# Kernel optimization log

Measured on AMD Instinct MI355X. Metric: run time of the kernel, lower is better.

## Reference

```python
import jax, jax.numpy as jnp
import numpy as np

N = 50000      # nodes
E = 400000     # edges (before self-loops)
F = 128        # num_features
H = 8          # heads
C = 64         # hidden_channels (per-head dim of conv1)
K = 32         # num_classes (per-head dim of conv2)
NEG_SLOPE = 0.2


def _glorot(key, shape):
    fan_in, fan_out = shape[0], shape[-1]
    scale = jnp.sqrt(2.0 / (fan_in + fan_out)).astype(jnp.float32)
    return jax.random.normal(key, shape, dtype=jnp.float32) * scale


def setup_inputs() -> dict:
    key = jax.random.key(0)
    ks = jax.random.split(key, 14)
    return {
        "x": jax.random.normal(ks[0], (N, F), dtype=jnp.float32),
        "edge_index": jax.random.randint(ks[1], (2, E), 0, N, dtype=jnp.int32),
        "xyz": jax.random.normal(ks[2], (N, 3), dtype=jnp.float32),
        # lin1 residual: Linear(F, K)
        "lin1_w": _glorot(ks[3], (F, K)),
        "lin1_b": jnp.zeros((K,), jnp.float32),
        # conv1: GATv2Conv(F, C, heads=8, concat=False)
        "wl1": _glorot(ks[4], (F, H * C)),
        "wr1": _glorot(ks[5], (F, H * C)),
        "att1": _glorot(ks[6], (H, C)),
        "b1": jnp.zeros((C,), jnp.float32),
        # conv2: GATv2Conv(C, K, heads=8, concat=False)
        "wl2": _glorot(ks[7], (C, H * K)),
        "wr2": _glorot(ks[8], (C, H * K)),
        "att2": _glorot(ks[9], (H, K)),
        "b2": jnp.zeros((K,), jnp.float32),
    }


def _gatv2_layer(x, src, dst, wl, wr, att, bias, heads, ch):
    """GATv2Conv with concat=False (mean over heads), add_self_loops already in edges."""
    n = x.shape[0]
    xl = (x @ wl).reshape(n, heads, ch)   # source transform W_l x
    xr = (x @ wr).reshape(n, heads, ch)   # target transform W_r x
    # edge score: e_ij = a_h . leaky_relu(xl[j] + xr[i])  -> [E, H]
    e = jnp.einsum('ehc,hc->eh', jax.nn.leaky_relu(xl[src] + xr[dst], NEG_SLOPE), att)
    # segment softmax over incoming edges of each destination node
    m = jax.ops.segment_max(e, dst, num_segments=n)
    ex = jnp.exp(e - m[dst])
    denom = jax.ops.segment_sum(ex, dst, num_segments=n)
    alpha = ex / denom[dst]                                      # [E, H]
    out = jax.ops.segment_sum(alpha[:, :, None] * xl[src], dst, num_segments=n)  # [N, H, C]
    return out.mean(axis=1) + bias        # concat=False -> head average, then bias


def reference(x, edge_index, xyz, lin1_w, lin1_b, wl1, wr1, att1, b1,
              wl2, wr2, att2, b2):
    n = x.shape[0]
    # PyG GATv2Conv default: add self loops
    loops = jnp.arange(n, dtype=edge_index.dtype)
    src = jnp.concatenate([edge_index[0], loops])
    dst = jnp.concatenate([edge_index[1], loops])

    residual1 = x @ lin1_w + lin1_b                      # lin1(x)
    h = _gatv2_layer(x, src, dst, wl1, wr1, att1, b1, H, C)
    h = jax.nn.relu(h)                                   # dropout is identity in eval
    out = _gatv2_layer(h, src, dst, wl2, wr2, att2, b2, H, K)
    return out + residual1
```

## Files before the change

### kernel.cpp

```cpp
#include <hip/hip_runtime.h>
#include <hip/hip_bf16.h>

#define NNODE 50000
#define NEDGE 400000
#define NTOT  450000
#define FDIM  128
#define HEADS 8
#define SCANB ((NNODE + 255) / 256)

typedef __bf16 bf16x8 __attribute__((ext_vector_type(8)));
typedef float  f32x4  __attribute__((ext_vector_type(4)));
typedef __hip_bfloat16 bf16;

static __device__ __forceinline__ float b2f(unsigned short u) {
  union { float f; unsigned int i; } x; x.i = ((unsigned int)u) << 16; return x.f;
}

template<int CTRL>
static __device__ __forceinline__ float dpp_add(float v) {
  int x = __builtin_amdgcn_update_dpp(0, __float_as_int(v), CTRL, 0xf, 0xf, true);
  return v + __int_as_float(x);
}


__global__ __launch_bounds__(256) void k_count(const int* __restrict__ ei, int* __restrict__ deg) {
  int t = blockIdx.x * 256 + threadIdx.x;
  if (t >= NTOT) return;
  int d = (t < NEDGE) ? ei[NEDGE + t] : (t - NEDGE);
  atomicAdd(&deg[d], 1);
}

__global__ __launch_bounds__(256) void k_scan1(const int* __restrict__ deg, int* __restrict__ offs,
                                               int* __restrict__ bsum) {
  __shared__ int buf[256];
  int i = blockIdx.x * 256 + threadIdx.x;
  int v = (i < NNODE) ? deg[i] : 0;
  buf[threadIdx.x] = v;
  __syncthreads();
  for (int off = 1; off < 256; off <<= 1) {
    int t = (threadIdx.x >= off) ? buf[threadIdx.x - off] : 0;
    __syncthreads();
    buf[threadIdx.x] += t;
    __syncthreads();
  }
  if (i < NNODE) offs[i + 1] = buf[threadIdx.x];
  if (threadIdx.x == 255) bsum[blockIdx.x] = buf[255];
  if (i == 0) offs[0] = 0;
}

__global__ __launch_bounds__(256) void k_scan2(int* __restrict__ bsum, int nb) {
  __shared__ int buf[256];
  int v = (threadIdx.x < nb) ? bsum[threadIdx.x] : 0;
  buf[threadIdx.x] = v;
  __syncthreads();
  for (int off = 1; off < 256; off <<= 1) {
    int t = (threadIdx.x >= off) ? buf[threadIdx.x - off] : 0;
    __syncthreads();
    buf[threadIdx.x] += t;
    __syncthreads();
  }
  if (threadIdx.x < nb) bsum[threadIdx.x] = buf[threadIdx.x] - v;
}

__global__ __launch_bounds__(256) void k_scan3(int* __restrict__ offs, const int* __restrict__ bsum) {
  int i = blockIdx.x * 256 + threadIdx.x;
  if (i < NNODE) offs[i + 1] += bsum[blockIdx.x];
}

__global__ __launch_bounds__(256) void k_fill(const int* __restrict__ ei, const int* __restrict__ offs,
                                              int* __restrict__ cur, int* __restrict__ csrc) {
  int t = blockIdx.x * 256 + threadIdx.x;
  if (t >= NTOT) return;
  int s, d;
  if (t < NEDGE) { s = ei[t]; d = ei[NEDGE + t]; }
  else { s = t - NEDGE; d = s; }
  int pos = offs[d] + atomicAdd(&cur[d], 1);
  csrc[pos] = s;
}


__global__ __launch_bounds__(256) void k_cast(const float* __restrict__ in, bf16* __restrict__ o, int nvec) {
  int t = blockIdx.x * 256 + threadIdx.x;
  if (t >= nvec) return;
  float4 v = *(const float4*)(in + (size_t)t * 4);
  bf16* p = o + (size_t)t * 4;
  p[0] = __float2bfloat16(v.x);
  p[1] = __float2bfloat16(v.y);
  p[2] = __float2bfloat16(v.z);
  p[3] = __float2bfloat16(v.w);
}


template<int K, int N>
__global__ __launch_bounds__(256) void k_pack(const float* __restrict__ Wl, const float* __restrict__ Wr,
                                              bf16* __restrict__ Bp) {
  constexpr int KS = K / 32;
  int t = blockIdx.x * 256 + threadIdx.x;
  if (t >= (N / 16) * KS * 64) return;
  int lane = t & 63;
  int ks = (t >> 6) % KS;
  int cb = t / (64 * KS);
  int col = cb * 16 + (lane & 15);
  int k0 = ks * 32 + (lane >> 4) * 8;
  const float* W = (col < N / 2) ? Wl : Wr;
  int c = (col < N / 2) ? col : col - N / 2;
  bf16* o = Bp + (size_t)t * 8;
#pragma unroll
  for (int j = 0; j < 8; ++j)
    o[j] = __float2bfloat16(W[(size_t)(k0 + j) * (N / 2) + c]);
}


template<int K, int N>
__global__ __launch_bounds__(256) void k_mfma(const bf16* __restrict__ A,
                                              const bf16* __restrict__ Bp,
                                              bf16* __restrict__ xl, bf16* __restrict__ xr,
                                              int n) {
  constexpr int KS = K / 32;
  const int lane = threadIdx.x & 63;
  const int wave = threadIdx.x >> 6;
  const int rb = blockIdx.x * 32;
  const int cb0 = blockIdx.y * 16 + wave * 4;
  const int r16 = lane & 15, kg = lane >> 4;

  bf16x8 a[2][KS];
#pragma unroll
  for (int mf = 0; mf < 2; ++mf) {
    int row = rb + 16 * mf + r16;
    if (row >= n) row = n - 1;
    const bf16* pa = A + (size_t)row * K + kg * 8;
#pragma unroll
    for (int ks = 0; ks < KS; ++ks)
      a[mf][ks] = *(const bf16x8*)(pa + ks * 32);
  }

#pragma unroll
  for (int nf = 0; nf < 4; ++nf) {
    int cb = cb0 + nf;
    f32x4 acc0 = {0.f, 0.f, 0.f, 0.f}, acc1 = {0.f, 0.f, 0.f, 0.f};
    const bf16* pb = Bp + (size_t)cb * KS * 512 + lane * 8;
#pragma unroll
    for (int ks = 0; ks < KS; ++ks) {
      bf16x8 b = *(const bf16x8*)(pb + ks * 512);
      acc0 = __builtin_amdgcn_mfma_f32_16x16x32_bf16(a[0][ks], b, acc0, 0, 0, 0);
      acc1 = __builtin_amdgcn_mfma_f32_16x16x32_bf16(a[1][ks], b, acc1, 0, 0, 0);
    }
    int col = cb * 16 + r16;
    bf16* OUT; int c;
    if (col < N / 2) { OUT = xl; c = col; } else { OUT = xr; c = col - N / 2; }
#pragma unroll
    for (int reg = 0; reg < 4; ++reg) {
      int row0 = rb + kg * 4 + reg;
      if (row0 < n) OUT[(size_t)row0 * (N / 2) + c] = __float2bfloat16(acc0[reg]);
      int row1 = rb + 16 + kg * 4 + reg;
      if (row1 < n) OUT[(size_t)row1 * (N / 2) + c] = __float2bfloat16(acc1[reg]);
    }
  }
}


__global__ __launch_bounds__(256) void k_residual(const float* __restrict__ X,
                                                  const float* __restrict__ W,
                                                  const float* __restrict__ b,
                                                  float* __restrict__ out, int n) {
  __shared__ float xs[8 * 128];
  int row0 = blockIdx.x * 8;
  for (int t = threadIdx.x; t < 8 * 128; t += 256) {
    int r = t >> 7;
    xs[t] = (row0 + r < n) ? X[(size_t)(row0 + r) * 128 + (t & 127)] : 0.f;
  }
  __syncthreads();
  int r = threadIdx.x >> 5, c = threadIdx.x & 31;
  float acc = 0.f;
  for (int k = 0; k < 128; ++k) acc += xs[r * 128 + k] * W[k * 32 + c];
  if (row0 + r < n) out[(size_t)(row0 + r) * 32 + c] = acc + b[c];
}


template<int D, int VEC, int W, bool L1>
__global__ __launch_bounds__(64 * W, 2) void k_gat(const bf16* __restrict__ xl,
                                                   const bf16* __restrict__ xr,
                                                   const float* __restrict__ att,
                                                   const int* __restrict__ csrc,
                                                   const int* __restrict__ offs,
                                                   const float* __restrict__ bias,
                                                   const float* __restrict__ resid,
                                                   bf16* __restrict__ out1,
                                                   float* __restrict__ out2) {
  constexpr int CH = D / 8;
  constexpr int NW = VEC / 2;
  constexpr unsigned ROWB = D * 2;
  typedef unsigned int uivec __attribute__((ext_vector_type(NW)));
  __shared__ float sden[W - 1][64];
  __shared__ float sacc[W - 1][64][VEC + 1];
  const int w    = threadIdx.x >> 6;
  const int lane = threadIdx.x & 63;
  const int node = blockIdx.x;
  const int beg = offs[node], end = offs[node + 1], last = end - 1;

  const unsigned loff = (unsigned)(lane * VEC) * 2u;
  const char* xlp = (const char*)xl + loff;

  float a6[VEC], a4[VEC], xrv[VEC];
  {
    const float* pa = att + lane * VEC;
    const unsigned int* rw = (const unsigned int*)((const char*)xr + (size_t)node * ROWB + loff);
#pragma unroll
    for (int p = 0; p < NW; ++p) {
      unsigned int rv = rw[p];
      xrv[2 * p]     = __uint_as_float(rv << 16);
      xrv[2 * p + 1] = __uint_as_float(rv & 0xffff0000u);
    }
#pragma unroll
    for (int j = 0; j < VEC; ++j) {
      float a = pa[j] * 1.44269504f;
      a6[j] = 0.6f * a;
      a4[j] = 0.4f * a;
    }
  }

  float den = 0.f;
  float acc[VEC];
#pragma unroll
  for (int j = 0; j < VEC; ++j) acc[j] = 0.f;

  auto escore = [&](uivec Wd, float* av) -> float {
    float s0 = 0.f, s1 = 0.f;
#pragma unroll
    for (int p = 0; p < NW; ++p) {
      av[2 * p]     = __uint_as_float(Wd[p] << 16);
      av[2 * p + 1] = __uint_as_float(Wd[p] & 0xffff0000u);
    }
#pragma unroll
    for (int j = 0; j < VEC; ++j) {
      float t = av[j] + xrv[j];
      s0 = fmaf(a6[j], t, s0);
      s1 = fmaf(a4[j], fabsf(t), s1);
    }
    return s0 + s1;
  };

  int i = beg + w;
  if (i < end) {
    uivec A0 = *(const uivec*)(xlp + (unsigned)csrc[i] * ROWB);
    int i1 = (i + W < end) ? i + W : last;
    uivec A1 = *(const uivec*)(xlp + (unsigned)csrc[i1] * ROWB);
    for (; i + W < end; i += 2 * W) {
      int i2 = (i + 2 * W < end) ? i + 2 * W : last;
      int i3 = (i + 3 * W < end) ? i + 3 * W : last;
      uivec B0 = *(const uivec*)(xlp + (unsigned)csrc[i2] * ROWB);
      uivec B1 = *(const uivec*)(xlp + (unsigned)csrc[i3] * ROWB);

      float av0[VEC], av1[VEC];
      float s0 = escore(A0, av0);
      float s1 = escore(A1, av1);
      s0 = dpp_add<0xB1>(s0);   s1 = dpp_add<0xB1>(s1);
      s0 = dpp_add<0x4E>(s0);   s1 = dpp_add<0x4E>(s1);
      s0 = dpp_add<0x141>(s0);  s1 = dpp_add<0x141>(s1);
      float w0, w1;
      asm("v_exp_f32 %0, %1" : "=v"(w0) : "v"(s0));
      asm("v_exp_f32 %0, %1" : "=v"(w1) : "v"(s1));
      den += w0;
      den += w1;
#pragma unroll
      for (int j = 0; j < VEC; ++j) {
        acc[j] = fmaf(w0, av0[j], acc[j]);
        acc[j] = fmaf(w1, av1[j], acc[j]);
      }
      A0 = B0; A1 = B1;
    }
    if (i < end) {
      float av0[VEC];
      float s0 = escore(A0, av0);
      s0 = dpp_add<0xB1>(s0);
      s0 = dpp_add<0x4E>(s0);
      s0 = dpp_add<0x141>(s0);
      float w0;
      asm("v_exp_f32 %0, %1" : "=v"(w0) : "v"(s0));
      den += w0;
#pragma unroll
      for (int j = 0; j < VEC; ++j) acc[j] = fmaf(w0, av0[j], acc[j]);
    }
  }

  if (w > 0) {
    sden[w - 1][lane] = den;
#pragma unroll
    for (int j = 0; j < VEC; ++j) sacc[w - 1][lane][j] = acc[j];
  }
  __syncthreads();
  if (w == 0) {
#pragma unroll
    for (int ww = 0; ww < W - 1; ++ww) {
      den += sden[ww][lane];
#pragma unroll
      for (int j = 0; j < VEC; ++j) acc[j] += sacc[ww][lane][j];
    }
    const float inv = 1.f / den;
    float v[VEC];
#pragma unroll
    for (int j = 0; j < VEC; ++j) {
      float t = acc[j] * inv;
      t += __shfl_xor(t, 8);
      t += __shfl_xor(t, 16);
      t += __shfl_xor(t, 32);
      v[j] = t;
    }
    if (lane < 8) {
      int c0 = lane * VEC;
      if constexpr (L1) {
        bf16* o = out1 + (size_t)node * CH + c0;
#pragma unroll
        for (int j = 0; j < VEC; ++j) {
          float t = v[j] * 0.125f + bias[c0 + j];
          o[j] = __float2bfloat16(fmaxf(t, 0.f));
        }
      } else {
        float* o = out2 + (size_t)node * CH + c0;
        const float* rs = resid + (size_t)node * CH + c0;
#pragma unroll
        for (int j = 0; j < VEC; ++j)
          o[j] = v[j] * 0.125f + bias[c0 + j] + rs[j];
      }
    }
  }
}


extern "C" void kernel_launch(void* const* d_in, const int* in_sizes, int n_in,
                              void* d_out, int out_size, void* d_ws, size_t ws_size,
                              hipStream_t stream) {
  const float* x      = (const float*)d_in[0];
  const int*   ei     = (const int*)d_in[1];
  const float* lin1_w = (const float*)d_in[3];
  const float* lin1_b = (const float*)d_in[4];
  const float* wl1    = (const float*)d_in[5];
  const float* wr1    = (const float*)d_in[6];
  const float* att1   = (const float*)d_in[7];
  const float* b1     = (const float*)d_in[8];
  const float* wl2    = (const float*)d_in[9];
  const float* wr2    = (const float*)d_in[10];
  const float* att2   = (const float*)d_in[11];
  const float* b2     = (const float*)d_in[12];
  float* out = (float*)d_out;

  char* p = (char*)d_ws;
  auto alloc = [&](size_t bytes) {
    char* r = p;
    p += (bytes + 255) & ~size_t(255);
    return r;
  };
  int*   offs  = (int*)alloc((NNODE + 1) * 4);
  int*   deg   = (int*)alloc(NNODE * 4);
  int*   cur   = (int*)alloc(NNODE * 4);
  int*   bsum  = (int*)alloc(SCANB * 4);
  int*   csrc  = (int*)alloc((size_t)NTOT * 4);
  bf16*  xb    = (bf16*)alloc((size_t)NNODE * 128 * 2);
  bf16*  xl    = (bf16*)alloc((size_t)NNODE * 512 * 2);
  bf16*  xr    = (bf16*)alloc((size_t)NNODE * 512 * 2);
  bf16*  h1    = (bf16*)alloc((size_t)NNODE * 64 * 2);
  bf16*  Bp1   = (bf16*)alloc((size_t)128 * 1024 * 2);
  bf16*  Bp2   = (bf16*)alloc((size_t)64 * 512 * 2);
  float* resid = (float*)alloc((size_t)NNODE * 32 * 4);

  (void)hipMemsetAsync(deg, 0, NNODE * 4, stream);
  (void)hipMemsetAsync(cur, 0, NNODE * 4, stream);

  k_count<<<(NTOT + 255) / 256, 256, 0, stream>>>(ei, deg);
  k_scan1<<<SCANB, 256, 0, stream>>>(deg, offs, bsum);
  k_scan2<<<1, 256, 0, stream>>>(bsum, SCANB);
  k_scan3<<<SCANB, 256, 0, stream>>>(offs, bsum);
  k_fill<<<(NTOT + 255) / 256, 256, 0, stream>>>(ei, offs, cur, csrc);
  k_cast<<<(NNODE * 128 / 4 + 255) / 256, 256, 0, stream>>>(x, xb, NNODE * 128 / 4);
  k_pack<128, 1024><<<64, 256, 0, stream>>>(wl1, wr1, Bp1);
  k_pack<64, 512><<<16, 256, 0, stream>>>(wl2, wr2, Bp2);
  k_residual<<<NNODE / 8, 256, 0, stream>>>(x, lin1_w, lin1_b, resid, NNODE);

  k_mfma<128, 1024><<<dim3((NNODE + 31) / 32, 4), 256, 0, stream>>>(xb, Bp1, xl, xr, NNODE);
  k_gat<512, 8, 4, true><<<NNODE, 256, 0, stream>>>(xl, xr, att1, csrc, offs, b1, nullptr, h1, nullptr);

  k_mfma<64, 512><<<dim3((NNODE + 31) / 32, 2), 256, 0, stream>>>(h1, Bp2, xl, xr, NNODE);
  k_gat<256, 4, 4, false><<<NNODE, 256, 0, stream>>>(xl, xr, att2, csrc, offs, b2, resid, nullptr, out);
}
```

Baseline: 292.5 us.

## Fuse fp32-to-bf16 cast into GEMM and simplify GAT edge-index prefetch

Removes the separate cast kernel and the bf16 copy of x, converting fp32 inputs to bf16 while loading GEMM A fragments. The GAT kernel now prefetches edge source indices several iterations ahead without clamping, relying on a zero-padded tail of the CSR source array for out-of-range reads. It also splits the score dot product into independent accumulators, vectorizes the conversion helpers, and raises the occupancy hint in launch bounds from 2 to 3. The first GEMM reads twice as many A bytes per tile, and the higher occupancy hint may force register spills.

```diff
diff --git a/kernel.cpp b/kernel.cpp
--- a/kernel.cpp
+++ b/kernel.cpp
@@ -7,14 +7,11 @@
 #define FDIM  128
 #define HEADS 8
 #define SCANB ((NNODE + 255) / 256)
+#define CSRC_PAD 256
 
 typedef __bf16 bf16x8 __attribute__((ext_vector_type(8)));
 typedef float  f32x4  __attribute__((ext_vector_type(4)));
 typedef __hip_bfloat16 bf16;
-
-static __device__ __forceinline__ float b2f(unsigned short u) {
-  union { float f; unsigned int i; } x; x.i = ((unsigned int)u) << 16; return x.f;
-}
 
 template<int CTRL>
 static __device__ __forceinline__ float dpp_add(float v) {
@@ -76,18 +73,6 @@
   else { s = t - NEDGE; d = s; }
   int pos = offs[d] + atomicAdd(&cur[d], 1);
   csrc[pos] = s;
-}
-
-
-__global__ __launch_bounds__(256) void k_cast(const float* __restrict__ in, bf16* __restrict__ o, int nvec) {
-  int t = blockIdx.x * 256 + threadIdx.x;
-  if (t >= nvec) return;
-  float4 v = *(const float4*)(in + (size_t)t * 4);
-  bf16* p = o + (size_t)t * 4;
-  p[0] = __float2bfloat16(v.x);
-  p[1] = __float2bfloat16(v.y);
-  p[2] = __float2bfloat16(v.z);
-  p[3] = __float2bfloat16(v.w);
 }
 
 
@@ -111,8 +96,8 @@
 }
 
 
-template<int K, int N>
-__global__ __launch_bounds__(256) void k_mfma(const bf16* __restrict__ A,
+template<int K, int N, bool CVT>
+__global__ __launch_bounds__(256) void k_mfma(const void* __restrict__ Aptr,
                                               const bf16* __restrict__ Bp,
                                               bf16* __restrict__ xl, bf16* __restrict__ xr,
                                               int n) {
@@ -128,10 +113,25 @@
   for (int mf = 0; mf < 2; ++mf) {
     int row = rb + 16 * mf + r16;
     if (row >= n) row = n - 1;
-    const bf16* pa = A + (size_t)row * K + kg * 8;
-#pragma unroll
-    for (int ks = 0; ks < KS; ++ks)
-      a[mf][ks] = *(const bf16x8*)(pa + ks * 32);
+    if constexpr (CVT) {
+      const float* pa = (const float*)Aptr + (size_t)row * K + kg * 8;
+#pragma unroll
+      for (int ks = 0; ks < KS; ++ks) {
+        float4 f0 = *(const float4*)(pa + ks * 32);
+        float4 f1 = *(const float4*)(pa + ks * 32 + 4);
+        bf16x8 v;
+        v[0] = __float2bfloat16(f0.x); v[1] = __float2bfloat16(f0.y);
+        v[2] = __float2bfloat16(f0.z); v[3] = __float2bfloat16(f0.w);
+        v[4] = __float2bfloat16(f1.x); v[5] = __float2bfloat16(f1.y);
+        v[6] = __float2bfloat16(f1.z); v[7] = __float2bfloat16(f1.w);
+        a[mf][ks] = v;
+      }
+    } else {
+      const bf16* pa = (const bf16*)Aptr + (size_t)row * K + kg * 8;
+#pragma unroll
+      for (int ks = 0; ks < KS; ++ks)
+        a[mf][ks] = *(const bf16x8*)(pa + ks * 32);
+    }
   }
 
 #pragma unroll
@@ -178,7 +178,7 @@
 
 
 template<int D, int VEC, int W, bool L1>
-__global__ __launch_bounds__(64 * W, 2) void k_gat(const bf16* __restrict__ xl,
+__global__ __launch_bounds__(64 * W, 3) void k_gat(const bf16* __restrict__ xl,
                                                    const bf16* __restrict__ xr,
                                                    const float* __restrict__ att,
                                                    const int* __restrict__ csrc,
@@ -191,26 +191,32 @@
   constexpr int NW = VEC / 2;
   constexpr unsigned ROWB = D * 2;
   typedef unsigned int uivec __attribute__((ext_vector_type(NW)));
+  typedef float fvec __attribute__((ext_vector_type(VEC)));
   __shared__ float sden[W - 1][64];
   __shared__ float sacc[W - 1][64][VEC + 1];
   const int w    = threadIdx.x >> 6;
   const int lane = threadIdx.x & 63;
   const int node = blockIdx.x;
-  const int beg = offs[node], end = offs[node + 1], last = end - 1;
+  const int beg = offs[node], end = offs[node + 1];
 
   const unsigned loff = (unsigned)(lane * VEC) * 2u;
   const char* xlp = (const char*)xl + loff;
 
-  float a6[VEC], a4[VEC], xrv[VEC];
+  auto cvt = [](uivec Wd) -> fvec {
+    fvec r;
+#pragma unroll
+    for (int p = 0; p < NW; ++p) {
+      r[2 * p]     = __uint_as_float(Wd[p] << 16);
+      r[2 * p + 1] = __uint_as_float(Wd[p] & 0xffff0000u);
+    }
+    return r;
+  };
+
+  fvec a6, a4, xrv;
   {
     const float* pa = att + lane * VEC;
-    const unsigned int* rw = (const unsigned int*)((const char*)xr + (size_t)node * ROWB + loff);
-#pragma unroll
-    for (int p = 0; p < NW; ++p) {
-      unsigned int rv = rw[p];
-      xrv[2 * p]     = __uint_as_float(rv << 16);
-      xrv[2 * p + 1] = __uint_as_float(rv & 0xffff0000u);
-    }
+    uivec rw = *(const uivec*)((const char*)xr + (size_t)node * ROWB + loff);
+    xrv = cvt(rw);
 #pragma unroll
     for (int j = 0; j < VEC; ++j) {
       float a = pa[j] * 1.44269504f;
@@ -220,40 +226,37 @@
   }
 
   float den = 0.f;
-  float acc[VEC];
+  fvec acc;
 #pragma unroll
   for (int j = 0; j < VEC; ++j) acc[j] = 0.f;
-
-  auto escore = [&](uivec Wd, float* av) -> float {
-    float s0 = 0.f, s1 = 0.f;
-#pragma unroll
-    for (int p = 0; p < NW; ++p) {
-      av[2 * p]     = __uint_as_float(Wd[p] << 16);
-      av[2 * p + 1] = __uint_as_float(Wd[p] & 0xffff0000u);
-    }
-#pragma unroll
-    for (int j = 0; j < VEC; ++j) {
-      float t = av[j] + xrv[j];
-      s0 = fmaf(a6[j], t, s0);
-      s1 = fmaf(a4[j], fabsf(t), s1);
-    }
-    return s0 + s1;
-  };
 
   int i = beg + w;
   if (i < end) {
-    uivec A0 = *(const uivec*)(xlp + (unsigned)csrc[i] * ROWB);
-    int i1 = (i + W < end) ? i + W : last;
-    uivec A1 = *(const uivec*)(xlp + (unsigned)csrc[i1] * ROWB);
+    int c0 = csrc[i];
+    int c1 = csrc[i + W];
+    int c2 = csrc[i + 2 * W];
+    int c3 = csrc[i + 3 * W];
+    uivec A0 = *(const uivec*)(xlp + (unsigned)c0 * ROWB);
+    uivec A1 = *(const uivec*)(xlp + (unsigned)c1 * ROWB);
     for (; i + W < end; i += 2 * W) {
-      int i2 = (i + 2 * W < end) ? i + 2 * W : last;
-      int i3 = (i + 3 * W < end) ? i + 3 * W : last;
-      uivec B0 = *(const uivec*)(xlp + (unsigned)csrc[i2] * ROWB);
-      uivec B1 = *(const uivec*)(xlp + (unsigned)csrc[i3] * ROWB);
-
-      float av0[VEC], av1[VEC];
-      float s0 = escore(A0, av0);
-      float s1 = escore(A1, av1);
+      uivec B0 = *(const uivec*)(xlp + (unsigned)c2 * ROWB);
+      uivec B1 = *(const uivec*)(xlp + (unsigned)c3 * ROWB);
+      c2 = csrc[i + 4 * W];
+      c3 = csrc[i + 5 * W];
+
+      fvec av0 = cvt(A0);
+      fvec av1 = cvt(A1);
+      fvec t0 = av0 + xrv;
+      fvec t1 = av1 + xrv;
+      float s0a = 0.f, s0b = 0.f, s1a = 0.f, s1b = 0.f;
+#pragma unroll
+      for (int j = 0; j < VEC; ++j) {
+        s0a = fmaf(a6[j], t0[j], s0a);
+        s0b = fmaf(a4[j], fabsf(t0[j]), s0b);
+        s1a = fmaf(a6[j], t1[j], s1a);
+        s1b = fmaf(a4[j], fabsf(t1[j]), s1b);
+      }
+      float s0 = s0a + s0b, s1 = s1a + s1b;
       s0 = dpp_add<0xB1>(s0);   s1 = dpp_add<0xB1>(s1);
       s0 = dpp_add<0x4E>(s0);   s1 = dpp_add<0x4E>(s1);
       s0 = dpp_add<0x141>(s0);  s1 = dpp_add<0x141>(s1);
@@ -270,8 +273,15 @@
       A0 = B0; A1 = B1;
     }
     if (i < end) {
-      float av0[VEC];
-      float s0 = escore(A0, av0);
+      fvec av0 = cvt(A0);
+      fvec t0 = av0 + xrv;
+      float s0a = 0.f, s0b = 0.f;
+#pragma unroll
+      for (int j = 0; j < VEC; ++j) {
+        s0a = fmaf(a6[j], t0[j], s0a);
+        s0b = fmaf(a4[j], fabsf(t0[j]), s0b);
+      }
+      float s0 = s0a + s0b;
       s0 = dpp_add<0xB1>(s0);
       s0 = dpp_add<0x4E>(s0);
       s0 = dpp_add<0x141>(s0);
@@ -297,7 +307,7 @@
       for (int j = 0; j < VEC; ++j) acc[j] += sacc[ww][lane][j];
     }
     const float inv = 1.f / den;
-    float v[VEC];
+    fvec v;
 #pragma unroll
     for (int j = 0; j < VEC; ++j) {
       float t = acc[j] * inv;
@@ -354,8 +364,7 @@
   int*   deg   = (int*)alloc(NNODE * 4);
   int*   cur   = (int*)alloc(NNODE * 4);
   int*   bsum  = (int*)alloc(SCANB * 4);
-  int*   csrc  = (int*)alloc((size_t)NTOT * 4);
-  bf16*  xb    = (bf16*)alloc((size_t)NNODE * 128 * 2);
+  int*   csrc  = (int*)alloc(((size_t)NTOT + CSRC_PAD) * 4);
   bf16*  xl    = (bf16*)alloc((size_t)NNODE * 512 * 2);
   bf16*  xr    = (bf16*)alloc((size_t)NNODE * 512 * 2);
   bf16*  h1    = (bf16*)alloc((size_t)NNODE * 64 * 2);
@@ -365,20 +374,20 @@
 
   (void)hipMemsetAsync(deg, 0, NNODE * 4, stream);
   (void)hipMemsetAsync(cur, 0, NNODE * 4, stream);
+  (void)hipMemsetAsync(csrc + NTOT, 0, CSRC_PAD * 4, stream);
 
   k_count<<<(NTOT + 255) / 256, 256, 0, stream>>>(ei, deg);
   k_scan1<<<SCANB, 256, 0, stream>>>(deg, offs, bsum);
   k_scan2<<<1, 256, 0, stream>>>(bsum, SCANB);
   k_scan3<<<SCANB, 256, 0, stream>>>(offs, bsum);
   k_fill<<<(NTOT + 255) / 256, 256, 0, stream>>>(ei, offs, cur, csrc);
-  k_cast<<<(NNODE * 128 / 4 + 255) / 256, 256, 0, stream>>>(x, xb, NNODE * 128 / 4);
   k_pack<128, 1024><<<64, 256, 0, stream>>>(wl1, wr1, Bp1);
   k_pack<64, 512><<<16, 256, 0, stream>>>(wl2, wr2, Bp2);
   k_residual<<<NNODE / 8, 256, 0, stream>>>(x, lin1_w, lin1_b, resid, NNODE);
 
-  k_mfma<128, 1024><<<dim3((NNODE + 31) / 32, 4), 256, 0, stream>>>(xb, Bp1, xl, xr, NNODE);
+  k_mfma<128, 1024, true><<<dim3((NNODE + 31) / 32, 4), 256, 0, stream>>>(x, Bp1, xl, xr, NNODE);
   k_gat<512, 8, 4, true><<<NNODE, 256, 0, stream>>>(xl, xr, att1, csrc, offs, b1, nullptr, h1, nullptr);
 
-  k_mfma<64, 512><<<dim3((NNODE + 31) / 32, 2), 256, 0, stream>>>(h1, Bp2, xl, xr, NNODE);
+  k_mfma<64, 512, false><<<dim3((NNODE + 31) / 32, 2), 256, 0, stream>>>(h1, Bp2, xl, xr, NNODE);
   k_gat<256, 4, 4, false><<<NNODE, 256, 0, stream>>>(xl, xr, att2, csrc, offs, b2, resid, nullptr, out);
 }
```

After: 326.6 us. 1.12x slower.

## Fuse fp32-to-bf16 cast into MFMA GEMM and precompute scaled attention vectors

Applied to the files above, without the earlier changes.

Removes the separate k_cast pass over x by having the layer-1 GEMM load fp32 rows and convert them to bf16 in registers. Doubles the column fragments each wave computes (NF=8), which halves the y-grid and reuses the loaded A rows across more output columns. Adds a tiny kernel that precomputes the log2e-scaled 0.6/0.4 attention coefficients, so the GAT kernels load them as vectors instead of recomputing them per block. The trade-off is higher register pressure in the GEMM and twice the A-read bandwidth in fp32 per block.

```diff
diff --git a/kernel.cpp b/kernel.cpp
--- a/kernel.cpp
+++ b/kernel.cpp
@@ -11,10 +11,6 @@
 typedef __bf16 bf16x8 __attribute__((ext_vector_type(8)));
 typedef float  f32x4  __attribute__((ext_vector_type(4)));
 typedef __hip_bfloat16 bf16;
-
-static __device__ __forceinline__ float b2f(unsigned short u) {
-  union { float f; unsigned int i; } x; x.i = ((unsigned int)u) << 16; return x.f;
-}
 
 template<int CTRL>
 static __device__ __forceinline__ float dpp_add(float v) {
@@ -79,15 +75,19 @@
 }
 
 
-__global__ __launch_bounds__(256) void k_cast(const float* __restrict__ in, bf16* __restrict__ o, int nvec) {
+__global__ __launch_bounds__(256) void k_attp(const float* __restrict__ att1, const float* __restrict__ att2,
+                                              float* __restrict__ attp1, float* __restrict__ attp2) {
   int t = blockIdx.x * 256 + threadIdx.x;
-  if (t >= nvec) return;
-  float4 v = *(const float4*)(in + (size_t)t * 4);
-  bf16* p = o + (size_t)t * 4;
-  p[0] = __float2bfloat16(v.x);
-  p[1] = __float2bfloat16(v.y);
-  p[2] = __float2bfloat16(v.z);
-  p[3] = __float2bfloat16(v.w);
+  if (t < 512) {
+    float a = att1[t] * 1.44269504f;
+    attp1[t] = 0.6f * a;
+    attp1[512 + t] = 0.4f * a;
+  } else if (t < 768) {
+    int c = t - 512;
+    float a = att2[c] * 1.44269504f;
+    attp2[c] = 0.6f * a;
+    attp2[256 + c] = 0.4f * a;
+  }
 }
 
 
@@ -111,8 +111,8 @@
 }
 
 
-template<int K, int N>
-__global__ __launch_bounds__(256) void k_mfma(const bf16* __restrict__ A,
+template<int K, int N, int NF, bool CVT>
+__global__ __launch_bounds__(256) void k_mfma(const void* __restrict__ Aptr,
                                               const bf16* __restrict__ Bp,
                                               bf16* __restrict__ xl, bf16* __restrict__ xr,
                                               int n) {
@@ -120,7 +120,7 @@
   const int lane = threadIdx.x & 63;
   const int wave = threadIdx.x >> 6;
   const int rb = blockIdx.x * 32;
-  const int cb0 = blockIdx.y * 16 + wave * 4;
+  const int cb0 = blockIdx.y * (4 * NF) + wave * NF;
   const int r16 = lane & 15, kg = lane >> 4;
 
   bf16x8 a[2][KS];
@@ -128,14 +128,29 @@
   for (int mf = 0; mf < 2; ++mf) {
     int row = rb + 16 * mf + r16;
     if (row >= n) row = n - 1;
-    const bf16* pa = A + (size_t)row * K + kg * 8;
-#pragma unroll
-    for (int ks = 0; ks < KS; ++ks)
-      a[mf][ks] = *(const bf16x8*)(pa + ks * 32);
-  }
-
-#pragma unroll
-  for (int nf = 0; nf < 4; ++nf) {
+    if constexpr (CVT) {
+      const float* pa = (const float*)Aptr + (size_t)row * K + kg * 8;
+#pragma unroll
+      for (int ks = 0; ks < KS; ++ks) {
+        float4 f0 = *(const float4*)(pa + ks * 32);
+        float4 f1 = *(const float4*)(pa + ks * 32 + 4);
+        bf16x8 v;
+        v[0] = __float2bfloat16(f0.x); v[1] = __float2bfloat16(f0.y);
+        v[2] = __float2bfloat16(f0.z); v[3] = __float2bfloat16(f0.w);
+        v[4] = __float2bfloat16(f1.x); v[5] = __float2bfloat16(f1.y);
+        v[6] = __float2bfloat16(f1.z); v[7] = __float2bfloat16(f1.w);
+        a[mf][ks] = v;
+      }
+    } else {
+      const bf16* pa = (const bf16*)Aptr + (size_t)row * K + kg * 8;
+#pragma unroll
+      for (int ks = 0; ks < KS; ++ks)
+        a[mf][ks] = *(const bf16x8*)(pa + ks * 32);
+    }
+  }
+
+#pragma unroll
+  for (int nf = 0; nf < NF; ++nf) {
     int cb = cb0 + nf;
     f32x4 acc0 = {0.f, 0.f, 0.f, 0.f}, acc1 = {0.f, 0.f, 0.f, 0.f};
     const bf16* pb = Bp + (size_t)cb * KS * 512 + lane * 8;
@@ -180,7 +195,7 @@
 template<int D, int VEC, int W, bool L1>
 __global__ __launch_bounds__(64 * W, 2) void k_gat(const bf16* __restrict__ xl,
                                                    const bf16* __restrict__ xr,
-                                                   const float* __restrict__ att,
+                                                   const float* __restrict__ attp,
                                                    const int* __restrict__ csrc,
                                                    const int* __restrict__ offs,
                                                    const float* __restrict__ bias,
@@ -191,6 +206,7 @@
   constexpr int NW = VEC / 2;
   constexpr unsigned ROWB = D * 2;
   typedef unsigned int uivec __attribute__((ext_vector_type(NW)));
+  typedef float fvec __attribute__((ext_vector_type(VEC)));
   __shared__ float sden[W - 1][64];
   __shared__ float sacc[W - 1][64][VEC + 1];
   const int w    = threadIdx.x >> 6;
@@ -201,30 +217,24 @@
   const unsigned loff = (unsigned)(lane * VEC) * 2u;
   const char* xlp = (const char*)xl + loff;
 
-  float a6[VEC], a4[VEC], xrv[VEC];
+  fvec a6 = *(const fvec*)(attp + lane * VEC);
+  fvec a4 = *(const fvec*)(attp + D + lane * VEC);
+  fvec xrv;
   {
-    const float* pa = att + lane * VEC;
-    const unsigned int* rw = (const unsigned int*)((const char*)xr + (size_t)node * ROWB + loff);
+    uivec rw = *(const uivec*)((const char*)xr + (size_t)node * ROWB + loff);
 #pragma unroll
     for (int p = 0; p < NW; ++p) {
-      unsigned int rv = rw[p];
-      xrv[2 * p]     = __uint_as_float(rv << 16);
-      xrv[2 * p + 1] = __uint_as_float(rv & 0xffff0000u);
-    }
-#pragma unroll
-    for (int j = 0; j < VEC; ++j) {
-      float a = pa[j] * 1.44269504f;
-      a6[j] = 0.6f * a;
-      a4[j] = 0.4f * a;
+      xrv[2 * p]     = __uint_as_float(rw[p] << 16);
+      xrv[2 * p + 1] = __uint_as_float(rw[p] & 0xffff0000u);
     }
   }
 
   float den = 0.f;
-  float acc[VEC];
+  fvec acc;
 #pragma unroll
   for (int j = 0; j < VEC; ++j) acc[j] = 0.f;
 
-  auto escore = [&](uivec Wd, float* av) -> float {
+  auto escore = [&](uivec Wd, fvec& av) -> float {
     float s0 = 0.f, s1 = 0.f;
 #pragma unroll
     for (int p = 0; p < NW; ++p) {
@@ -251,7 +261,7 @@
       uivec B0 = *(const uivec*)(xlp + (unsigned)csrc[i2] * ROWB);
       uivec B1 = *(const uivec*)(xlp + (unsigned)csrc[i3] * ROWB);
 
-      float av0[VEC], av1[VEC];
+      fvec av0, av1;
       float s0 = escore(A0, av0);
       float s1 = escore(A1, av1);
       s0 = dpp_add<0xB1>(s0);   s1 = dpp_add<0xB1>(s1);
@@ -270,7 +280,7 @@
       A0 = B0; A1 = B1;
     }
     if (i < end) {
-      float av0[VEC];
+      fvec av0;
       float s0 = escore(A0, av0);
       s0 = dpp_add<0xB1>(s0);
       s0 = dpp_add<0x4E>(s0);
@@ -297,7 +307,7 @@
       for (int j = 0; j < VEC; ++j) acc[j] += sacc[ww][lane][j];
     }
     const float inv = 1.f / den;
-    float v[VEC];
+    fvec v;
 #pragma unroll
     for (int j = 0; j < VEC; ++j) {
       float t = acc[j] * inv;
@@ -355,12 +365,13 @@
   int*   cur   = (int*)alloc(NNODE * 4);
   int*   bsum  = (int*)alloc(SCANB * 4);
   int*   csrc  = (int*)alloc((size_t)NTOT * 4);
-  bf16*  xb    = (bf16*)alloc((size_t)NNODE * 128 * 2);
   bf16*  xl    = (bf16*)alloc((size_t)NNODE * 512 * 2);
   bf16*  xr    = (bf16*)alloc((size_t)NNODE * 512 * 2);
   bf16*  h1    = (bf16*)alloc((size_t)NNODE * 64 * 2);
   bf16*  Bp1   = (bf16*)alloc((size_t)128 * 1024 * 2);
   bf16*  Bp2   = (bf16*)alloc((size_t)64 * 512 * 2);
+  float* attp1 = (float*)alloc(1024 * 4);
+  float* attp2 = (float*)alloc(512 * 4);
   float* resid = (float*)alloc((size_t)NNODE * 32 * 4);
 
   (void)hipMemsetAsync(deg, 0, NNODE * 4, stream);
@@ -371,14 +382,14 @@
   k_scan2<<<1, 256, 0, stream>>>(bsum, SCANB);
   k_scan3<<<SCANB, 256, 0, stream>>>(offs, bsum);
   k_fill<<<(NTOT + 255) / 256, 256, 0, stream>>>(ei, offs, cur, csrc);
-  k_cast<<<(NNODE * 128 / 4 + 255) / 256, 256, 0, stream>>>(x, xb, NNODE * 128 / 4);
+  k_attp<<<3, 256, 0, stream>>>(att1, att2, attp1, attp2);
   k_pack<128, 1024><<<64, 256, 0, stream>>>(wl1, wr1, Bp1);
   k_pack<64, 512><<<16, 256, 0, stream>>>(wl2, wr2, Bp2);
   k_residual<<<NNODE / 8, 256, 0, stream>>>(x, lin1_w, lin1_b, resid, NNODE);
 
-  k_mfma<128, 1024><<<dim3((NNODE + 31) / 32, 4), 256, 0, stream>>>(xb, Bp1, xl, xr, NNODE);
-  k_gat<512, 8, 4, true><<<NNODE, 256, 0, stream>>>(xl, xr, att1, csrc, offs, b1, nullptr, h1, nullptr);
-
-  k_mfma<64, 512><<<dim3((NNODE + 31) / 32, 2), 256, 0, stream>>>(h1, Bp2, xl, xr, NNODE);
-  k_gat<256, 4, 4, false><<<NNODE, 256, 0, stream>>>(xl, xr, att2, csrc, offs, b2, resid, nullptr, out);
-}
+  k_mfma<128, 1024, 8, true><<<dim3((NNODE + 31) / 32, 2), 256, 0, stream>>>(x, Bp1, xl, xr, NNODE);
+  k_gat<512, 8, 4, true><<<NNODE, 256, 0, stream>>>(xl, xr, attp1, csrc, offs, b1, nullptr, h1, nullptr);
+
+  k_mfma<64, 512, 8, false><<<dim3((NNODE + 31) / 32, 1), 256, 0, stream>>>(h1, Bp2, xl, xr, NNODE);
+  k_gat<256, 4, 4, false><<<NNODE, 256, 0, stream>>>(xl, xr, attp2, csrc, offs, b2, resid, nullptr, out);
+}
```

Result: slower. 323.0 us (+10.5%).
